# Kernel optimization log

Measured on AMD Instinct MI355X. Metric: run time of the kernel, lower is better.

Reference implementation:

```python
import math
import jax, jax.numpy as jnp
import numpy as np

B, S, D, H = 2, 2048, 1024, 16
HD = D // H  # head_dim = 64


def setup_inputs() -> dict:
    key = jax.random.key(0)
    k1, k2, k3 = jax.random.split(key, 3)
    scale = 0.02
    return {
        "x": jax.random.normal(k1, (B, S, D), dtype=jnp.float32),
        "w_qkv": jax.random.normal(k2, (D, 3 * D), dtype=jnp.float32) * scale,
        "b_qkv": jnp.zeros((3 * D,), dtype=jnp.float32),
        "w_proj": jax.random.normal(k3, (D, D), dtype=jnp.float32) * scale,
        "b_proj": jnp.zeros((D,), dtype=jnp.float32),
    }


def reference(x, w_qkv, b_qkv, w_proj, b_proj):
    bsz, seq_len, d_model = x.shape
    # fused qkv projection: [B,S,3D] -> [3,B,H,S,HD]
    qkv = (x @ w_qkv + b_qkv).reshape(bsz, seq_len, 3, H, HD)
    qkv = jnp.transpose(qkv, (2, 0, 3, 1, 4))
    q, k, v = qkv[0], qkv[1], qkv[2]
    # scores [B,H,S,S]
    scores = jnp.einsum("bhqd,bhkd->bhqk", q, k) / math.sqrt(HD)
    causal = jnp.tril(jnp.ones((seq_len, seq_len), dtype=bool))
    scores = jnp.where(causal[None, None], scores, -jnp.inf)
    probs = jax.nn.softmax(scores, axis=-1)
    # dropout = 0.0 (eval mode)
    context = jnp.einsum("bhqk,bhkd->bhqd", probs, v)
    context = jnp.transpose(context, (0, 2, 1, 3)).reshape(bsz, seq_len, d_model)
    return context @ w_proj + b_proj
```

## Files before the change

kernel.cpp:

```cpp
#include <hip/hip_runtime.h>

#define B_ 2
#define S_ 2048
#define D_ 1024
#define H_ 16
#define HD_ 64
#define M_ (B_*S_)
#define N_QKV (3*D_)

typedef __attribute__((ext_vector_type(8))) short short8;
typedef __attribute__((ext_vector_type(4))) float floatx4;

__device__ __forceinline__ float fast_exp2(float x) {
    return __builtin_amdgcn_exp2f(x);
}

__device__ __forceinline__ unsigned short f2b(float f) {
    union { float f; unsigned int u; } v; v.f = f;
    unsigned int u = v.u;
    u += 0x7FFFu + ((u >> 16) & 1u);
    return (unsigned short)(u >> 16);
}
__device__ __forceinline__ unsigned short f2b_fast(float f) {
    union { float f; unsigned int u; } v; v.f = f;
    return (unsigned short)((v.u + 0x8000u) >> 16);
}

__device__ __forceinline__ void glds16(const unsigned short* g, unsigned short* lds) {
    __builtin_amdgcn_global_load_lds(
        (const __attribute__((address_space(1))) unsigned int*)g,
        (__attribute__((address_space(3))) unsigned int*)lds, 16, 0, 0);
}

__global__ __launch_bounds__(256) void prep_kernel(
    const float* __restrict__ x,      unsigned short* __restrict__ xb,
    const float* __restrict__ w_qkv,  unsigned short* __restrict__ wqkvT,
    const float* __restrict__ w_proj, unsigned short* __restrict__ wprojT)
{
    __shared__ float tile[32][33];
    const int id = blockIdx.x;
    if (id < 4096) {
        const int i = (id * 256 + threadIdx.x) * 4;
        float4 f = *(const float4*)(x + i);
        ushort4 o;
        o.x = f2b(f.x); o.y = f2b(f.y); o.z = f2b(f.z); o.w = f2b(f.w);
        *(ushort4*)(xb + i) = o;
    } else {
        const float* W; unsigned short* Wt; int cols, bx, by;
        if (id < 4096 + 3072) {
            W = w_qkv; Wt = wqkvT; cols = N_QKV;
            const int r = id - 4096; bx = r % 96; by = r / 96;
        } else {
            W = w_proj; Wt = wprojT; cols = D_;
            const int r = id - 7168; bx = r % 32; by = r / 32;
        }
        const int rows = D_;
        const int tx = threadIdx.x & 31, ty = threadIdx.x >> 5;
        const int c0 = bx * 32, r0 = by * 32;
        #pragma unroll
        for (int i = 0; i < 4; ++i)
            tile[ty + i*8][tx] = W[(size_t)(r0 + ty + i*8) * cols + c0 + tx];
        __syncthreads();
        #pragma unroll
        for (int i = 0; i < 4; ++i)
            Wt[(size_t)(c0 + ty + i*8) * rows + r0 + tx] = f2b(tile[tx][ty + i*8]);
    }
}

__global__ __launch_bounds__(256, 3) void gemm_bt_kernel(
    const unsigned short* __restrict__ A,
    const unsigned short* __restrict__ Bt,
    const float* __restrict__ bias,
    unsigned short* __restrict__ q,
    unsigned short* __restrict__ k_,
    unsigned short* __restrict__ vt,
    int Kdim)
{
    __shared__ unsigned short SMEM[128*136];
    unsigned short* As = SMEM;
    unsigned short* Bs = SMEM + 128*64;

    const int t = threadIdx.x;
    const int lane = t & 63;
    const int w = t >> 6;
    const int wm = w >> 1, wn = w & 1;
    const int quad = lane >> 4, l15 = lane & 15;
    const int bm = blockIdx.y, bn = blockIdx.x;

    const int sr32 = t >> 3;
    const int gch  = (t & 7) ^ (sr32 & 7);

    const unsigned short* gA = A  + (size_t)(bm*128 + sr32) * Kdim + gch*8;
    const unsigned short* gB = Bt + (size_t)(bn*128 + sr32) * Kdim + gch*8;
    const size_t rstep = (size_t)32 * Kdim;

    unsigned short* lA = As + (w*8)*64;
    unsigned short* lB = Bs + (w*8)*64;

    const int swz = (l15 & 7);

    auto stage_g = [&](int kk) {
        #pragma unroll
        for (int c = 0; c < 4; ++c) {
            glds16(gA + c*rstep + kk, lA + c*2048);
            glds16(gB + c*rstep + kk, lB + c*2048);
        }
    };

    floatx4 acc[4][4];
    #pragma unroll
    for (int i = 0; i < 4; ++i)
        #pragma unroll
        for (int j = 0; j < 4; ++j)
            acc[i][j] = (floatx4){0.f, 0.f, 0.f, 0.f};

    stage_g(0);
    for (int k0 = 0; k0 < Kdim; k0 += 64) {
        __syncthreads();
        short8 an[4][2], am[4][2];
        #pragma unroll
        for (int i = 0; i < 4; ++i)
            #pragma unroll
            for (int kk = 0; kk < 2; ++kk) {
                const int coff = ((quad + 4*kk) ^ swz) * 8;
                an[i][kk] = *(const short8*)&Bs[(wn*64 + i*16 + l15)*64 + coff];
                am[i][kk] = *(const short8*)&As[(wm*64 + i*16 + l15)*64 + coff];
            }
        __syncthreads();
        if (k0 + 64 < Kdim) stage_g(k0 + 64);
        #pragma unroll
        for (int kk = 0; kk < 2; ++kk)
            #pragma unroll
            for (int i = 0; i < 4; ++i)
                #pragma unroll
                for (int j = 0; j < 4; ++j)
                    acc[i][j] = __builtin_amdgcn_mfma_f32_16x16x32_bf16(an[i][kk], am[j][kk], acc[i][j], 0, 0, 0);
    }

    const float QSCALE = 0.18033688011112042f;
    const int which = bn >> 3;
    const int hcol  = (bn & 7)*2 + wn;
    const int b     = bm >> 4;
    const int sbase0 = (bm & 15)*128;
    const int sbase  = sbase0 + wm*64;

    if (which == 2) {
        unsigned short (*L)[136] = (unsigned short (*)[136])SMEM;
        #pragma unroll
        for (int i = 0; i < 4; ++i) {
            float4 bias4 = *(const float4*)&bias[bn*128 + wn*64 + i*16 + quad*4];
            const int n0 = wn*64 + i*16 + quad*4;
            #pragma unroll
            for (int j = 0; j < 4; ++j) {
                const int m = wm*64 + j*16 + l15;
                L[n0+0][m] = f2b(acc[i][j][0] + bias4.x);
                L[n0+1][m] = f2b(acc[i][j][1] + bias4.y);
                L[n0+2][m] = f2b(acc[i][j][2] + bias4.z);
                L[n0+3][m] = f2b(acc[i][j][3] + bias4.w);
            }
        }
        __syncthreads();
        const int r = t >> 1, half = t & 1;
        const int hcr = (bn & 7)*2 + (r >> 6);
        const int hdr = r & 63;
        unsigned short* dst = &vt[(((size_t)(b*H_ + hcr))*HD_ + hdr)*S_ + sbase0 + half*64];
        const unsigned short* srcL = &L[r][half*64];
        #pragma unroll
        for (int c = 0; c < 8; ++c)
            *(uint4*)&dst[c*8] = *(const uint4*)&srcL[c*8];
    } else {
        #pragma unroll
        for (int i = 0; i < 4; ++i) {
            float4 bias4 = *(const float4*)&bias[bn*128 + wn*64 + i*16 + quad*4];
            const int hd0 = i*16 + quad*4;
            #pragma unroll
            for (int j = 0; j < 4; ++j) {
                const int srow = sbase + j*16 + l15;
                float v0 = acc[i][j][0] + bias4.x;
                float v1 = acc[i][j][1] + bias4.y;
                float v2 = acc[i][j][2] + bias4.z;
                float v3 = acc[i][j][3] + bias4.w;
                if (which == 0) {
                    v0 *= QSCALE; v1 *= QSCALE; v2 *= QSCALE; v3 *= QSCALE;
                    ushort4 o; o.x = f2b(v0); o.y = f2b(v1); o.z = f2b(v2); o.w = f2b(v3);
                    *(ushort4*)&q[((size_t)(b*H_ + hcol) * S_ + srow) * HD_ + hd0] = o;
                } else {
                    ushort4 o; o.x = f2b(v0); o.y = f2b(v1); o.z = f2b(v2); o.w = f2b(v3);
                    *(ushort4*)&k_[((size_t)(b*H_ + hcol) * S_ + srow) * HD_ + hd0] = o;
                }
            }
        }
    }
}

__global__ __launch_bounds__(256, 2) void gemm_bt64_kernel(
    const unsigned short* __restrict__ A,
    const unsigned short* __restrict__ Bt,
    const float* __restrict__ bias,
    float* __restrict__ outf,
    int Ndim, int Kdim)
{
    __shared__ unsigned short As[128*64];
    __shared__ unsigned short Bs[64*64];

    const int t = threadIdx.x;
    const int lane = t & 63;
    const int w = t >> 6;
    const int quad = lane >> 4, l15 = lane & 15;
    const int bm = blockIdx.y, bn = blockIdx.x;

    const int sr32 = t >> 3;
    const int gch  = (t & 7) ^ (sr32 & 7);

    const unsigned short* gA = A  + (size_t)(bm*128 + sr32) * Kdim + gch*8;
    const unsigned short* gB = Bt + (size_t)(bn*64  + sr32) * Kdim + gch*8;
    const size_t rstep = (size_t)32 * Kdim;

    unsigned short* lA = As + (w*8)*64;
    unsigned short* lB = Bs + (w*8)*64;

    const int swz = (l15 & 7);

    auto stage_g = [&](int kk) {
        #pragma unroll
        for (int c = 0; c < 4; ++c)
            glds16(gA + c*rstep + kk, lA + c*2048);
        #pragma unroll
        for (int c = 0; c < 2; ++c)
            glds16(gB + c*rstep + kk, lB + c*2048);
    };

    floatx4 acc[4][2];
    #pragma unroll
    for (int i = 0; i < 4; ++i)
        #pragma unroll
        for (int j = 0; j < 2; ++j)
            acc[i][j] = (floatx4){0.f, 0.f, 0.f, 0.f};

    stage_g(0);
    for (int k0 = 0; k0 < Kdim; k0 += 64) {
        __syncthreads();
        short8 an[4][2], am[2][2];
        #pragma unroll
        for (int kk = 0; kk < 2; ++kk) {
            const int coff = ((quad + 4*kk) ^ swz) * 8;
            #pragma unroll
            for (int i = 0; i < 4; ++i)
                an[i][kk] = *(const short8*)&Bs[(i*16 + l15)*64 + coff];
            #pragma unroll
            for (int j = 0; j < 2; ++j)
                am[j][kk] = *(const short8*)&As[(w*32 + j*16 + l15)*64 + coff];
        }
        __syncthreads();
        if (k0 + 64 < Kdim) stage_g(k0 + 64);
        #pragma unroll
        for (int kk = 0; kk < 2; ++kk)
            #pragma unroll
            for (int i = 0; i < 4; ++i)
                #pragma unroll
                for (int j = 0; j < 2; ++j)
                    acc[i][j] = __builtin_amdgcn_mfma_f32_16x16x32_bf16(an[i][kk], am[j][kk], acc[i][j], 0, 0, 0);
    }

    #pragma unroll
    for (int i = 0; i < 4; ++i) {
        float4 bias4 = *(const float4*)&bias[bn*64 + i*16 + quad*4];
        #pragma unroll
        for (int j = 0; j < 2; ++j) {
            const int gm = bm*128 + w*32 + j*16 + l15;
            float4 o;
            o.x = acc[i][j][0] + bias4.x;
            o.y = acc[i][j][1] + bias4.y;
            o.z = acc[i][j][2] + bias4.z;
            o.w = acc[i][j][3] + bias4.w;
            *(float4*)&outf[(size_t)gm * Ndim + bn*64 + i*16 + quad*4] = o;
        }
    }
}

__global__ __launch_bounds__(256, 2) void attn_kernel(
    const unsigned short* __restrict__ Q,
    const unsigned short* __restrict__ K,
    const unsigned short* __restrict__ Vt,
    unsigned short* __restrict__ ctx)
{
    __shared__ unsigned short KVs[2][2][64*64];
    __shared__ unsigned short Pt[4][2][16][72];

    const int t = threadIdx.x;
    const int lane = t & 63, w = t >> 6;
    const int quad = lane >> 4, l15 = lane & 15;
    const int bh = blockIdx.x & 31;
    const int a  = blockIdx.x >> 5;
    const int Hc = 31 - a;
    const int Lc = a;

    const unsigned short* Qh  = Q  + (size_t)bh * S_ * HD_;
    const unsigned short* Kh  = K  + (size_t)bh * S_ * HD_;
    const unsigned short* Vth = Vt + (size_t)bh * HD_ * S_;

    const int sr = t >> 3, sc = t & 7;
    const int gch = sc ^ (sr & 7);

    auto stage = [&](int j, int d) {
        unsigned short* kb = &KVs[d][0][0];
        unsigned short* vb = &KVs[d][1][0];
        const unsigned short* gk = Kh  + (size_t)(j*64 + sr)*HD_ + gch*8;
        const unsigned short* gv = Vth + (size_t)sr*S_ + (size_t)j*64 + gch*8;
        glds16(gk,                  kb + (w*8)*64);
        glds16(gk + 32*HD_,         kb + (32 + w*8)*64);
        glds16(gv,                  vb + (w*8)*64);
        glds16(gv + (size_t)32*S_,  vb + (32 + w*8)*64);
    };

    const int qH = Hc*64 + w*16;
    const int qL = Lc*64 + w*16;

    short8 bqH[2], bqL[2];
    #pragma unroll
    for (int kk = 0; kk < 2; ++kk) {
        bqH[kk] = *(const short8*)&Qh[(size_t)(qH + l15)*HD_ + kk*32 + quad*8];
        bqL[kk] = *(const short8*)&Qh[(size_t)(qL + l15)*HD_ + kk*32 + quad*8];
    }

    floatx4 OH[4], OL[4];
    #pragma unroll
    for (int nb = 0; nb < 4; ++nb) {
        OH[nb] = (floatx4){0.f,0.f,0.f,0.f};
        OL[nb] = (floatx4){0.f,0.f,0.f,0.f};
    }
    float lH = 0.f, lL = 0.f;

    stage(0, 0);

    for (int j = 0; j <= Hc; ++j) {
        __syncthreads();
        if (j < Hc) stage(j+1, (j+1)&1);
        const int d = j & 1;
        const unsigned short* Ksb = &KVs[d][0][0];
        const unsigned short* Vsb = &KVs[d][1][0];
        const bool doL = (j <= Lc);

        short8 ak[4][2], av[4][2];
        #pragma unroll
        for (int nb = 0; nb < 4; ++nb)
            #pragma unroll
            for (int kk = 0; kk < 2; ++kk) {
                int off = (nb*16 + l15)*64 + (((quad + 4*kk) ^ (l15 & 7)) * 8);
                ak[nb][kk] = *(const short8*)&Ksb[off];
                av[nb][kk] = *(const short8*)&Vsb[off];
            }

        float zH[4][4], zL[4][4];
        __builtin_amdgcn_s_setprio(1);
        #pragma unroll
        for (int nb = 0; nb < 4; ++nb) {
            floatx4 c = (floatx4){0.f,0.f,0.f,0.f};
            c = __builtin_amdgcn_mfma_f32_16x16x32_bf16(ak[nb][0], bqH[0], c, 0,0,0);
            c = __builtin_amdgcn_mfma_f32_16x16x32_bf16(ak[nb][1], bqH[1], c, 0,0,0);
            #pragma unroll
            for (int r = 0; r < 4; ++r) zH[nb][r] = c[r];
        }
        if (doL) {
            #pragma unroll
            for (int nb = 0; nb < 4; ++nb) {
                floatx4 c = (floatx4){0.f,0.f,0.f,0.f};
                c = __builtin_amdgcn_mfma_f32_16x16x32_bf16(ak[nb][0], bqL[0], c, 0,0,0);
                c = __builtin_amdgcn_mfma_f32_16x16x32_bf16(ak[nb][1], bqL[1], c, 0,0,0);
                #pragma unroll
                for (int r = 0; r < 4; ++r) zL[nb][r] = c[r];
            }
        }
        __builtin_amdgcn_s_setprio(0);

        if (j == Hc) {
            const int qg = qH + l15, koff = j*64;
            #pragma unroll
            for (int nb = 0; nb < 4; ++nb)
                #pragma unroll
                for (int r = 0; r < 4; ++r)
                    if (koff + nb*16 + quad*4 + r > qg) zH[nb][r] = -1e30f;
        }
        if (doL && j == Lc) {
            const int qg = qL + l15, koff = j*64;
            #pragma unroll
            for (int nb = 0; nb < 4; ++nb)
                #pragma unroll
                for (int r = 0; r < 4; ++r)
                    if (koff + nb*16 + quad*4 + r > qg) zL[nb][r] = -1e30f;
        }

        {
            float rs = 0.f;
            #pragma unroll
            for (int nb = 0; nb < 4; ++nb) {
                float p0 = fast_exp2(zH[nb][0]);
                float p1 = fast_exp2(zH[nb][1]);
                float p2 = fast_exp2(zH[nb][2]);
                float p3 = fast_exp2(zH[nb][3]);
                rs += (p0 + p1) + (p2 + p3);
                ushort4 pk;
                pk.x = f2b_fast(p0); pk.y = f2b_fast(p1);
                pk.z = f2b_fast(p2); pk.w = f2b_fast(p3);
                *(ushort4*)&Pt[w][0][l15][nb*16 + quad*4] = pk;
            }
            lH += rs;
        }
        if (doL) {
            float rs = 0.f;
            #pragma unroll
            for (int nb = 0; nb < 4; ++nb) {
                float p0 = fast_exp2(zL[nb][0]);
                float p1 = fast_exp2(zL[nb][1]);
                float p2 = fast_exp2(zL[nb][2]);
                float p3 = fast_exp2(zL[nb][3]);
                rs += (p0 + p1) + (p2 + p3);
                ushort4 pk;
                pk.x = f2b_fast(p0); pk.y = f2b_fast(p1);
                pk.z = f2b_fast(p2); pk.w = f2b_fast(p3);
                *(ushort4*)&Pt[w][1][l15][nb*16 + quad*4] = pk;
            }
            lL += rs;
        }

        short8 bpH0 = *(const short8*)&Pt[w][0][l15][quad*8];
        short8 bpH1 = *(const short8*)&Pt[w][0][l15][32 + quad*8];
        __builtin_amdgcn_s_setprio(1);
        #pragma unroll
        for (int nb = 0; nb < 4; ++nb) {
            OH[nb] = __builtin_amdgcn_mfma_f32_16x16x32_bf16(av[nb][0], bpH0, OH[nb], 0,0,0);
            OH[nb] = __builtin_amdgcn_mfma_f32_16x16x32_bf16(av[nb][1], bpH1, OH[nb], 0,0,0);
        }
        __builtin_amdgcn_s_setprio(0);
        if (doL) {
            short8 bpL0 = *(const short8*)&Pt[w][1][l15][quad*8];
            short8 bpL1 = *(const short8*)&Pt[w][1][l15][32 + quad*8];
            __builtin_amdgcn_s_setprio(1);
            #pragma unroll
            for (int nb = 0; nb < 4; ++nb) {
                OL[nb] = __builtin_amdgcn_mfma_f32_16x16x32_bf16(av[nb][0], bpL0, OL[nb], 0,0,0);
                OL[nb] = __builtin_amdgcn_mfma_f32_16x16x32_bf16(av[nb][1], bpL1, OL[nb], 0,0,0);
            }
            __builtin_amdgcn_s_setprio(0);
        }
    }

    const int b = bh >> 4, h = bh & (H_ - 1);
    auto finish = [&](floatx4 (&O)[4], float l_acc, int qbase) {
        l_acc += __shfl_xor(l_acc, 16, 64);
        l_acc += __shfl_xor(l_acc, 32, 64);
        const float inv = 1.f / l_acc;
        const int qg = qbase + l15;
        #pragma unroll
        for (int nb = 0; nb < 4; ++nb) {
            ushort4 o;
            o.x = f2b(O[nb][0] * inv);
            o.y = f2b(O[nb][1] * inv);
            o.z = f2b(O[nb][2] * inv);
            o.w = f2b(O[nb][3] * inv);
            *(ushort4*)&ctx[((size_t)(b*S_ + qg))*D_ + h*HD_ + nb*16 + quad*4] = o;
        }
    };
    finish(OH, lH, qH);
    finish(OL, lL, qL);
}

extern "C" void kernel_launch(void* const* d_in, const int* in_sizes, int n_in,
                              void* d_out, int out_size, void* d_ws, size_t ws_size,
                              hipStream_t stream) {
    const float* x      = (const float*)d_in[0];
    const float* w_qkv  = (const float*)d_in[1];
    const float* b_qkv  = (const float*)d_in[2];
    const float* w_proj = (const float*)d_in[3];
    const float* b_proj = (const float*)d_in[4];
    float* out = (float*)d_out;

    unsigned short* xb     = (unsigned short*)d_ws;
    unsigned short* wqkvT  = xb     + (size_t)M_ * D_;
    unsigned short* wprojT = wqkvT  + (size_t)N_QKV * D_;
    unsigned short* Qb     = wprojT + (size_t)D_ * D_;
    unsigned short* Kb     = Qb     + (size_t)B_*H_*S_*HD_;
    unsigned short* Vb     = Kb     + (size_t)B_*H_*S_*HD_;
    unsigned short* Vtb    = Vb     + (size_t)B_*H_*S_*HD_;
    unsigned short* ctx    = xb;

    prep_kernel<<<dim3(8192), dim3(256), 0, stream>>>(x, xb, w_qkv, wqkvT, w_proj, wprojT);

    gemm_bt_kernel<<<dim3(N_QKV/128, M_/128), dim3(256), 0, stream>>>(
        xb, wqkvT, b_qkv, Qb, Kb, Vtb, D_);

    attn_kernel<<<dim3(512), dim3(256), 0, stream>>>(Qb, Kb, Vtb, ctx);

    gemm_bt64_kernel<<<dim3(D_/64, M_/128), dim3(256), 0, stream>>>(
        ctx, wprojT, b_proj, out, D_, D_);
}
```

Before: 169.7 us.

## Pair adjacent query tiles per attention block instead of head/tail balancing

Each attention block previously processed two query tiles from opposite ends of the sequence (one high, one low) so that causal work per block was balanced. It now processes two adjacent 64-row tiles, so the K/V loop length varies from 2 to 32 tiles per block, and blocks are launched longest-first. Launch bounds are also raised from 2 to 3 blocks per CU to increase occupancy. This cuts the total K/V tiles staged per block, since adjacent tiles share nearly all keys, but introduces per-block load imbalance and may cause register spills under the tighter register budget.

```diff
diff --git a/kernel.cpp b/kernel.cpp
--- a/kernel.cpp
+++ b/kernel.cpp
@@ -278,7 +278,7 @@
     }
 }
 
-__global__ __launch_bounds__(256, 2) void attn_kernel(
+__global__ __launch_bounds__(256, 3) void attn_kernel(
     const unsigned short* __restrict__ Q,
     const unsigned short* __restrict__ K,
     const unsigned short* __restrict__ Vt,
@@ -291,9 +291,8 @@
     const int lane = t & 63, w = t >> 6;
     const int quad = lane >> 4, l15 = lane & 15;
     const int bh = blockIdx.x & 31;
-    const int a  = blockIdx.x >> 5;
-    const int Hc = 31 - a;
-    const int Lc = a;
+    const int c  = 15 - (blockIdx.x >> 5);
+    const int jmax = 2*c + 1;
 
     const unsigned short* Qh  = Q  + (size_t)bh * S_ * HD_;
     const unsigned short* Kh  = K  + (size_t)bh * S_ * HD_;
@@ -313,33 +312,33 @@
         glds16(gv + (size_t)32*S_,  vb + (32 + w*8)*64);
     };
 
-    const int qH = Hc*64 + w*16;
-    const int qL = Lc*64 + w*16;
-
-    short8 bqH[2], bqL[2];
+    const int q0 = c*128 + w*16;
+    const int q1 = q0 + 64;
+
+    short8 bq0[2], bq1[2];
     #pragma unroll
     for (int kk = 0; kk < 2; ++kk) {
-        bqH[kk] = *(const short8*)&Qh[(size_t)(qH + l15)*HD_ + kk*32 + quad*8];
-        bqL[kk] = *(const short8*)&Qh[(size_t)(qL + l15)*HD_ + kk*32 + quad*8];
-    }
-
-    floatx4 OH[4], OL[4];
+        bq0[kk] = *(const short8*)&Qh[(size_t)(q0 + l15)*HD_ + kk*32 + quad*8];
+        bq1[kk] = *(const short8*)&Qh[(size_t)(q1 + l15)*HD_ + kk*32 + quad*8];
+    }
+
+    floatx4 O0[4], O1[4];
     #pragma unroll
     for (int nb = 0; nb < 4; ++nb) {
-        OH[nb] = (floatx4){0.f,0.f,0.f,0.f};
-        OL[nb] = (floatx4){0.f,0.f,0.f,0.f};
-    }
-    float lH = 0.f, lL = 0.f;
+        O0[nb] = (floatx4){0.f,0.f,0.f,0.f};
+        O1[nb] = (floatx4){0.f,0.f,0.f,0.f};
+    }
+    float l0 = 0.f, l1 = 0.f;
 
     stage(0, 0);
 
-    for (int j = 0; j <= Hc; ++j) {
-        __syncthreads();
-        if (j < Hc) stage(j+1, (j+1)&1);
+    for (int j = 0; j <= jmax; ++j) {
+        __syncthreads();
+        if (j < jmax) stage(j+1, (j+1)&1);
         const int d = j & 1;
         const unsigned short* Ksb = &KVs[d][0][0];
         const unsigned short* Vsb = &KVs[d][1][0];
-        const bool doL = (j <= Lc);
+        const bool do0 = (j <= 2*c);
 
         short8 ak[4][2], av[4][2];
         #pragma unroll
@@ -351,98 +350,98 @@
                 av[nb][kk] = *(const short8*)&Vsb[off];
             }
 
-        float zH[4][4], zL[4][4];
+        float z0[4][4], z1[4][4];
         __builtin_amdgcn_s_setprio(1);
+        if (do0) {
+            #pragma unroll
+            for (int nb = 0; nb < 4; ++nb) {
+                floatx4 cc = (floatx4){0.f,0.f,0.f,0.f};
+                cc = __builtin_amdgcn_mfma_f32_16x16x32_bf16(ak[nb][0], bq0[0], cc, 0,0,0);
+                cc = __builtin_amdgcn_mfma_f32_16x16x32_bf16(ak[nb][1], bq0[1], cc, 0,0,0);
+                #pragma unroll
+                for (int r = 0; r < 4; ++r) z0[nb][r] = cc[r];
+            }
+        }
         #pragma unroll
         for (int nb = 0; nb < 4; ++nb) {
-            floatx4 c = (floatx4){0.f,0.f,0.f,0.f};
-            c = __builtin_amdgcn_mfma_f32_16x16x32_bf16(ak[nb][0], bqH[0], c, 0,0,0);
-            c = __builtin_amdgcn_mfma_f32_16x16x32_bf16(ak[nb][1], bqH[1], c, 0,0,0);
-            #pragma unroll
-            for (int r = 0; r < 4; ++r) zH[nb][r] = c[r];
-        }
-        if (doL) {
-            #pragma unroll
-            for (int nb = 0; nb < 4; ++nb) {
-                floatx4 c = (floatx4){0.f,0.f,0.f,0.f};
-                c = __builtin_amdgcn_mfma_f32_16x16x32_bf16(ak[nb][0], bqL[0], c, 0,0,0);
-                c = __builtin_amdgcn_mfma_f32_16x16x32_bf16(ak[nb][1], bqL[1], c, 0,0,0);
-                #pragma unroll
-                for (int r = 0; r < 4; ++r) zL[nb][r] = c[r];
-            }
+            floatx4 cc = (floatx4){0.f,0.f,0.f,0.f};
+            cc = __builtin_amdgcn_mfma_f32_16x16x32_bf16(ak[nb][0], bq1[0], cc, 0,0,0);
+            cc = __builtin_amdgcn_mfma_f32_16x16x32_bf16(ak[nb][1], bq1[1], cc, 0,0,0);
+            #pragma unroll
+            for (int r = 0; r < 4; ++r) z1[nb][r] = cc[r];
         }
         __builtin_amdgcn_s_setprio(0);
 
-        if (j == Hc) {
-            const int qg = qH + l15, koff = j*64;
+        if (j == 2*c) {
+            const int qg = q0 + l15, koff = j*64;
             #pragma unroll
             for (int nb = 0; nb < 4; ++nb)
                 #pragma unroll
                 for (int r = 0; r < 4; ++r)
-                    if (koff + nb*16 + quad*4 + r > qg) zH[nb][r] = -1e30f;
-        }
-        if (doL && j == Lc) {
-            const int qg = qL + l15, koff = j*64;
+                    if (koff + nb*16 + quad*4 + r > qg) z0[nb][r] = -1e30f;
+        }
+        if (j == jmax) {
+            const int qg = q1 + l15, koff = j*64;
             #pragma unroll
             for (int nb = 0; nb < 4; ++nb)
                 #pragma unroll
                 for (int r = 0; r < 4; ++r)
-                    if (koff + nb*16 + quad*4 + r > qg) zL[nb][r] = -1e30f;
-        }
-
-        {
+                    if (koff + nb*16 + quad*4 + r > qg) z1[nb][r] = -1e30f;
+        }
+
+        if (do0) {
             float rs = 0.f;
             #pragma unroll
             for (int nb = 0; nb < 4; ++nb) {
-                float p0 = fast_exp2(zH[nb][0]);
-                float p1 = fast_exp2(zH[nb][1]);
-                float p2 = fast_exp2(zH[nb][2]);
-                float p3 = fast_exp2(zH[nb][3]);
+                float p0 = fast_exp2(z0[nb][0]);
+                float p1 = fast_exp2(z0[nb][1]);
+                float p2 = fast_exp2(z0[nb][2]);
+                float p3 = fast_exp2(z0[nb][3]);
                 rs += (p0 + p1) + (p2 + p3);
                 ushort4 pk;
                 pk.x = f2b_fast(p0); pk.y = f2b_fast(p1);
                 pk.z = f2b_fast(p2); pk.w = f2b_fast(p3);
                 *(ushort4*)&Pt[w][0][l15][nb*16 + quad*4] = pk;
             }
-            lH += rs;
-        }
-        if (doL) {
+            l0 += rs;
+        }
+        {
             float rs = 0.f;
             #pragma unroll
             for (int nb = 0; nb < 4; ++nb) {
-                float p0 = fast_exp2(zL[nb][0]);
-                float p1 = fast_exp2(zL[nb][1]);
-                float p2 = fast_exp2(zL[nb][2]);
-                float p3 = fast_exp2(zL[nb][3]);
+                float p0 = fast_exp2(z1[nb][0]);
+                float p1 = fast_exp2(z1[nb][1]);
+                float p2 = fast_exp2(z1[nb][2]);
+                float p3 = fast_exp2(z1[nb][3]);
                 rs += (p0 + p1) + (p2 + p3);
                 ushort4 pk;
                 pk.x = f2b_fast(p0); pk.y = f2b_fast(p1);
                 pk.z = f2b_fast(p2); pk.w = f2b_fast(p3);
                 *(ushort4*)&Pt[w][1][l15][nb*16 + quad*4] = pk;
             }
-            lL += rs;
-        }
-
-        short8 bpH0 = *(const short8*)&Pt[w][0][l15][quad*8];
-        short8 bpH1 = *(const short8*)&Pt[w][0][l15][32 + quad*8];
+            l1 += rs;
+        }
+
         __builtin_amdgcn_s_setprio(1);
-        #pragma unroll
-        for (int nb = 0; nb < 4; ++nb) {
-            OH[nb] = __builtin_amdgcn_mfma_f32_16x16x32_bf16(av[nb][0], bpH0, OH[nb], 0,0,0);
-            OH[nb] = __builtin_amdgcn_mfma_f32_16x16x32_bf16(av[nb][1], bpH1, OH[nb], 0,0,0);
+        if (do0) {
+            short8 bp0 = *(const short8*)&Pt[w][0][l15][quad*8];
+            short8 bp1 = *(const short8*)&Pt[w][0][l15][32 + quad*8];
+            #pragma unroll
+            for (int nb = 0; nb < 4; ++nb) {
+                O0[nb] = __builtin_amdgcn_mfma_f32_16x16x32_bf16(av[nb][0], bp0, O0[nb], 0,0,0);
+                O0[nb] = __builtin_amdgcn_mfma_f32_16x16x32_bf16(av[nb][1], bp1, O0[nb], 0,0,0);
+            }
+        }
+        {
+            short8 bp0 = *(const short8*)&Pt[w][1][l15][quad*8];
+            short8 bp1 = *(const short8*)&Pt[w][1][l15][32 + quad*8];
+            #pragma unroll
+            for (int nb = 0; nb < 4; ++nb) {
+                O1[nb] = __builtin_amdgcn_mfma_f32_16x16x32_bf16(av[nb][0], bp0, O1[nb], 0,0,0);
+                O1[nb] = __builtin_amdgcn_mfma_f32_16x16x32_bf16(av[nb][1], bp1, O1[nb], 0,0,0);
+            }
         }
         __builtin_amdgcn_s_setprio(0);
-        if (doL) {
-            short8 bpL0 = *(const short8*)&Pt[w][1][l15][quad*8];
-            short8 bpL1 = *(const short8*)&Pt[w][1][l15][32 + quad*8];
-            __builtin_amdgcn_s_setprio(1);
-            #pragma unroll
-            for (int nb = 0; nb < 4; ++nb) {
-                OL[nb] = __builtin_amdgcn_mfma_f32_16x16x32_bf16(av[nb][0], bpL0, OL[nb], 0,0,0);
-                OL[nb] = __builtin_amdgcn_mfma_f32_16x16x32_bf16(av[nb][1], bpL1, OL[nb], 0,0,0);
-            }
-            __builtin_amdgcn_s_setprio(0);
-        }
     }
 
     const int b = bh >> 4, h = bh & (H_ - 1);
@@ -461,8 +460,8 @@
             *(ushort4*)&ctx[((size_t)(b*S_ + qg))*D_ + h*HD_ + nb*16 + quad*4] = o;
         }
     };
-    finish(OH, lH, qH);
-    finish(OL, lL, qL);
+    finish(O0, l0, q0);
+    finish(O1, l1, q1);
 }
 
 extern "C" void kernel_launch(void* const* d_in, const int* in_sizes, int n_in,
```

Measured after the change: 177.8 us. 4.8% more time.
